# Kernel tuning notes

Hardware: AMD Instinct MI355X
Metric: run time of the kernel (lower is better)

Reference implementation:

```python
import jax, jax.numpy as jnp
import numpy as np

MAX_DEPTH = 9
HIDDEN = 64
EMB = 64
POS_FREQS = 6
IN_C = 1
SIZES = [4 ** d for d in range(MAX_DEPTH + 1)]
OFFSETS = np.concatenate([[0], np.cumsum(SIZES)])  # per-depth slices into concatenated node arrays
TOTAL = int(OFFSETS[-1])  # 349525
POS_DIM = 3 + 2 * POS_FREQS * 3  # 39


def _interleave(v):
    v = v & 0xFFFF
    v = (v | (v << 8)) & 0x00FF00FF
    v = (v | (v << 4)) & 0x0F0F0F0F
    v = (v | (v << 2)) & 0x33333333
    v = (v | (v << 1)) & 0x55555555
    return v


def _deinterleave(v):
    v = v & 0x55555555
    v = (v | (v >> 1)) & 0x33333333
    v = (v | (v >> 2)) & 0x0F0F0F0F
    v = (v | (v >> 4)) & 0x00FF00FF
    v = (v | (v >> 8)) & 0x0000FFFF
    return v


def _xy(d):
    keys = jnp.arange(4 ** d, dtype=jnp.int32)  # full tree: sorted Morton keys = arange
    return _deinterleave(keys), _deinterleave(keys >> 1)


def _neighbors(d):
    # [N, 9] neighbor indices in Morton order grid; -1 outside the image (matches quadtree.neighs padding)
    ix, iy = _xy(d)
    res = 1 << d
    cols = []
    for dy in (-1, 0, 1):
        for dx in (-1, 0, 1):
            nx, ny = ix + dx, iy + dy
            valid = (nx >= 0) & (nx < res) & (ny >= 0) & (ny < res)
            key = _interleave(nx) | (_interleave(ny) << 1)
            cols.append(jnp.where(valid, key, -1))
    return jnp.stack(cols, axis=1)


def _pos_enc(d):
    # node_centers_from_keys + fourier_encode
    ix, iy = _xy(d)
    res = float(1 << d)
    x = (ix.astype(jnp.float32) + 0.5) / res
    y = (iy.astype(jnp.float32) + 0.5) / res
    dn = jnp.full_like(x, float(d) / float(MAX_DEPTH))
    pos = jnp.stack([x, y, dn], axis=1)  # [N, 3]
    freqs = 2.0 ** jnp.arange(POS_FREQS, dtype=jnp.float32)
    ang = pos[:, :, None] * (2.0 * np.pi) * freqs  # [N, 3, F]
    enc = jnp.concatenate([jnp.sin(ang), jnp.cos(ang)], axis=-1).reshape(pos.shape[0], -1)  # [N, 3*2F]
    return jnp.concatenate([pos, enc], axis=1)  # [N, 39]


def setup_inputs() -> dict:
    key = jax.random.key(0)
    ks = jax.random.split(key, 10)
    s = 0.05
    return {
        "features_in": jax.random.normal(ks[0], (TOTAL, IN_C), jnp.float32),
        "in_proj_W": jax.random.normal(ks[1], (IN_C + POS_DIM, HIDDEN), jnp.float32) * s,
        "in_proj_b": jnp.zeros((HIDDEN,), jnp.float32),
        "conv_W": jax.random.normal(ks[2], (MAX_DEPTH + 1, 9 * HIDDEN, HIDDEN), jnp.float32) * s,
        "conv_b": jnp.zeros((MAX_DEPTH + 1, HIDDEN), jnp.float32),
        "emb_W": jax.random.normal(ks[3], (MAX_DEPTH + 1, HIDDEN, EMB), jnp.float32) * s,
        "emb_b": jnp.zeros((MAX_DEPTH + 1, EMB), jnp.float32),
        "ln_g": jnp.ones((MAX_DEPTH + 1, EMB), jnp.float32),
        "ln_b": jnp.zeros((MAX_DEPTH + 1, EMB), jnp.float32),
        "depth_gain": jnp.ones((MAX_DEPTH + 1,), jnp.float32),
    }


def reference(features_in, in_proj_W, in_proj_b, conv_W, conv_b, emb_W, emb_b, ln_g, ln_b, depth_gain):
    D = MAX_DEPTH
    # per-depth input projection with fourier positional encoding
    h = []
    for d in range(D + 1):
        f = features_in[OFFSETS[d]:OFFSETS[d + 1]]
        x = jnp.concatenate([f, _pos_enc(d)], axis=1)  # [N_d, in_c + 39]
        h.append(x @ in_proj_W + in_proj_b)
    # bottom-up: QuadPool (mean over 4 children; full tree => children of parent i are 4i..4i+3) + QuadConv
    for d in range(D, 0, -1):
        Np = 4 ** (d - 1)
        pooled = h[d].reshape(Np, 4, HIDDEN).mean(axis=1)
        hd1 = h[d - 1] + pooled
        if d - 1 >= 1:
            neigh = _neighbors(d - 1)  # [N, 9], -1 at borders
            N = neigh.shape[0]
            padded = jnp.concatenate([hd1, jnp.zeros((1, HIDDEN), hd1.dtype)], axis=0)
            gi = jnp.where(neigh < 0, N, neigh)
            col = padded[gi].reshape(N, 9 * HIDDEN)
            hd1 = jax.nn.relu(col @ conv_W[d - 1] + conv_b[d - 1])
        h[d - 1] = hd1
    # per-depth embedding head: Linear -> LayerNorm -> depth gain
    outs = []
    eps = 1e-5
    for d in range(D + 1):
        z = h[d] @ emb_W[d] + emb_b[d]
        mu = z.mean(-1, keepdims=True)
        var = ((z - mu) ** 2).mean(-1, keepdims=True)
        z = (z - mu) / jnp.sqrt(var + eps) * ln_g[d] + ln_b[d]
        outs.append(depth_gain[d] * z)
    return jnp.concatenate(outs, axis=0)  # [TOTAL, EMB] (E[0]..E[max_depth] concatenated)
```

## Files before the change

kernel.cpp:

```cpp
#include <hip/hip_runtime.h>
#include <hip/hip_bf16.h>

static constexpr int TOTAL = 349525;
static constexpr int OFFS[11] = {0,1,5,21,85,341,1365,5461,21845,87381,349525};
static constexpr size_t CONV_USH = (size_t)8*9*2*4*64*8;
static constexpr size_t EMB_USH  = (size_t)10*2*4*64*8;
static constexpr size_t FRAG_USH = CONV_USH + EMB_USH;
static constexpr size_t FRAG_BYTES = FRAG_USH*2*2;
static constexpr size_t HPRE_BYTES = (size_t)(87381-85)*64*4;
static constexpr int WPREP_BLOCKS = 164;
static constexpr int INPROJ_BLOCKS = (TOTAL + 127)/128;

typedef __attribute__((ext_vector_type(8))) short short8;
typedef __attribute__((ext_vector_type(4))) float f32x4;

__device__ __forceinline__ unsigned deint(unsigned v){
  v &= 0x55555555u;
  v = (v | (v>>1)) & 0x33333333u;
  v = (v | (v>>2)) & 0x0F0F0F0Fu;
  v = (v | (v>>4)) & 0x00FF00FFu;
  v = (v | (v>>8)) & 0x0000FFFFu;
  return v;
}
__device__ __forceinline__ unsigned ileave(unsigned v){
  v &= 0xFFFFu;
  v = (v | (v<<8)) & 0x00FF00FFu;
  v = (v | (v<<4)) & 0x0F0F0F0Fu;
  v = (v | (v<<2)) & 0x33333333u;
  v = (v | (v<<1)) & 0x55555555u;
  return v;
}
__device__ __forceinline__ unsigned short f2bh(float x){
  unsigned u = __float_as_uint(x);
  return (unsigned short)((u + 0x7FFFu + ((u>>16)&1u)) >> 16);
}
__device__ __forceinline__ float bh2f(unsigned short h){
  return __uint_as_float(((unsigned)h) << 16);
}
__device__ __forceinline__ void split8(float4 a, float4 b, short8 &hi, short8 &lo){
  float v[8] = {a.x,a.y,a.z,a.w,b.x,b.y,b.z,b.w};
  unsigned short hv[8], lv[8];
  #pragma unroll
  for (int j=0;j<8;++j){ hv[j]=f2bh(v[j]); lv[j]=f2bh(v[j]-bh2f(hv[j])); }
  hi = short8{(short)hv[0],(short)hv[1],(short)hv[2],(short)hv[3],
              (short)hv[4],(short)hv[5],(short)hv[6],(short)hv[7]};
  lo = short8{(short)lv[0],(short)lv[1],(short)lv[2],(short)lv[3],
              (short)lv[4],(short)lv[5],(short)lv[6],(short)lv[7]};
}

__global__ __launch_bounds__(256) void k_prep(const float* __restrict__ convW,
    const float* __restrict__ embW,
    unsigned short* __restrict__ WH, unsigned short* __restrict__ WLo,
    const float* __restrict__ feat, const float* __restrict__ ipW,
    const float* __restrict__ ipB, float* __restrict__ h,
    float* __restrict__ hpre){
  __shared__ float Alt[128][44];
  __shared__ float Wl[40][68];
  int t = threadIdx.x;
  if ((int)blockIdx.x < WPREP_BLOCKS){
    int tid = blockIdx.x*256 + t;
    if (tid >= 41984) return;
    const float* src;
    size_t dst;
    if (tid < 36864){
      int l=tid&63, cb=(tid>>6)&3, ks=(tid>>8)&1;
      int x=tid>>9; int m=x%9, Lp=x/9;
      int k0=ks*32+((l>>4)<<3), ch=cb*16+(l&15);
      src = convW + (size_t)(Lp+1)*36864 + (size_t)(m*64+k0)*64 + ch;
      dst = (size_t)tid*8;
    } else {
      int t2 = tid - 36864;
      int l=t2&63, cb=(t2>>6)&3, ks=(t2>>8)&1, d=t2>>9;
      int k0=ks*32+((l>>4)<<3), ch=cb*16+(l&15);
      src = embW + (size_t)d*4096 + (size_t)k0*64 + ch;
      dst = CONV_USH + (size_t)t2*8;
    }
    unsigned short hv[8], lv[8];
    #pragma unroll
    for (int j=0;j<8;++j){
      float v = src[(size_t)j*64];
      unsigned short hh = f2bh(v);
      hv[j] = hh;
      lv[j] = f2bh(v - bh2f(hh));
    }
    short8 vh = {(short)hv[0],(short)hv[1],(short)hv[2],(short)hv[3],
                 (short)hv[4],(short)hv[5],(short)hv[6],(short)hv[7]};
    short8 vl = {(short)lv[0],(short)lv[1],(short)lv[2],(short)lv[3],
                 (short)lv[4],(short)lv[5],(short)lv[6],(short)lv[7]};
    *(short8*)(WH  + dst) = vh;
    *(short8*)(WLo + dst) = vl;
    return;
  }
  int base = ((int)blockIdx.x - WPREP_BLOCKS) * 128;
  for (int idx = t; idx < 40*64; idx += 256)
    Wl[idx >> 6][idx & 63] = ipW[idx];
  if (t < 128){
    int g = base + t;
    float* row = Alt[t];
    if (g < TOTAL){
      int d = 0;
      #pragma unroll
      for (int i = 1; i <= 9; ++i) if (g >= OFFS[i]) d = i;
      int local = g - OFFS[d];
      unsigned ix = deint((unsigned)local), iy = deint(((unsigned)local) >> 1);
      float inv = 1.0f / (float)(1 << d);
      float px = ((float)ix + 0.5f) * inv;
      float py = ((float)iy + 0.5f) * inv;
      float pd = (float)d * (1.0f/9.0f);
      row[0] = feat[g]; row[1] = px; row[2] = py; row[3] = pd;
      float p3[3] = {px, py, pd};
      #pragma unroll
      for (int c = 0; c < 3; ++c){
        float s, co;
        __sincosf(6.28318530717958647692f * p3[c], &s, &co);
        float* rb = row + 4 + c*12;
        #pragma unroll
        for (int f = 0; f < 6; ++f){
          rb[f] = s; rb[6+f] = co;
          float s2 = 2.f*s*co, c2 = 1.f - 2.f*s*s;
          s = s2; co = c2;
        }
      }
    } else {
      #pragma unroll
      for (int k = 0; k < 40; ++k) row[k] = 0.f;
    }
  }
  __syncthreads();
  int tr = t >> 3, tc = t & 7;
  float acc[4][8];
  #pragma unroll
  for (int i=0;i<4;++i)
    #pragma unroll
    for (int c=0;c<8;++c) acc[i][c] = 0.f;
  #pragma unroll 2
  for (int k4 = 0; k4 < 10; ++k4){
    float av4[4][4];
    #pragma unroll
    for (int i=0;i<4;++i){
      float4 aa = *(const float4*)&Alt[tr*4+i][k4*4];
      av4[i][0]=aa.x; av4[i][1]=aa.y; av4[i][2]=aa.z; av4[i][3]=aa.w;
    }
    #pragma unroll
    for (int j=0;j<4;++j){
      float4 lo = *(const float4*)&Wl[k4*4+j][tc*8];
      float4 hi = *(const float4*)&Wl[k4*4+j][tc*8+4];
      float wv[8];
      wv[0]=lo.x; wv[1]=lo.y; wv[2]=lo.z; wv[3]=lo.w;
      wv[4]=hi.x; wv[5]=hi.y; wv[6]=hi.z; wv[7]=hi.w;
      #pragma unroll
      for (int i=0;i<4;++i){
        float a = av4[i][j];
        #pragma unroll
        for (int c=0;c<8;++c) acc[i][c] += a*wv[c];
      }
    }
  }
  #pragma unroll
  for (int i=0;i<4;++i){
    int g = base + tr*4 + i;
    if (g >= TOTAL) continue;
    float ov[8];
    #pragma unroll
    for (int c=0;c<8;++c) ov[c] = acc[i][c] + ipB[tc*8+c];
    float* dst = &h[(size_t)g*64 + tc*8];
    *(float4*)dst       = *(const float4*)&ov[0];
    *(float4*)(dst + 4) = *(const float4*)&ov[4];
    if (hpre && g >= OFFS[4] && g < OFFS[9]){
      float* dp = hpre + (size_t)(g - OFFS[4])*64 + tc*8;
      *(float4*)dp       = *(const float4*)&ov[0];
      *(float4*)(dp + 4) = *(const float4*)&ov[4];
    }
  }
}

__device__ __forceinline__ void conv_dev(float* __restrict__ h,
    const float* __restrict__ hPar,
    const unsigned short* __restrict__ WHl, const unsigned short* __restrict__ WLl,
    const float* __restrict__ Bb, int N, int offL, int offC, int lbits, int bnum,
    unsigned short* haloH, unsigned short* haloL, int* hkey, int t){
  int nb = bnum * 64;
  int res = 1 << lbits;
  if (t < 100){
    int i = t % 10, j = t / 10;
    int gx = (int)deint((unsigned)nb) - 1 + i;
    int gy = (int)deint(((unsigned)nb)>>1) - 1 + j;
    bool ok = (gx>=0 && gy>=0 && gx<res && gy<res);
    hkey[t] = ok ? (int)(ileave((unsigned)gx) | (ileave((unsigned)gy)<<1)) : -1;
  }
  __syncthreads();
  const float* hC = h + (size_t)offC*64;
  for (int e = t; e < 1600; e += 256){
    int hi_ = e >> 4, u = e & 15;
    int key = hkey[hi_];
    float4 r = make_float4(0.f,0.f,0.f,0.f);
    if (key >= 0){
      const float4* c = (const float4*)(hC + (size_t)(4*key)*64) + u;
      float4 c0 = c[0], c1 = c[16], c2 = c[32], c3 = c[48];
      float4 pr = *((const float4*)(hPar + (size_t)key*64) + u);
      r.x = 0.25f*(c0.x+c1.x+c2.x+c3.x) + pr.x;
      r.y = 0.25f*(c0.y+c1.y+c2.y+c3.y) + pr.y;
      r.z = 0.25f*(c0.z+c1.z+c2.z+c3.z) + pr.z;
      r.w = 0.25f*(c0.w+c1.w+c2.w+c3.w) + pr.w;
    }
    unsigned short h0=f2bh(r.x), h1=f2bh(r.y), h2=f2bh(r.z), h3=f2bh(r.w);
    *(ushort4*)&haloH[hi_*72 + u*4] = make_ushort4(h0,h1,h2,h3);
    *(ushort4*)&haloL[hi_*72 + u*4] = make_ushort4(
        f2bh(r.x - bh2f(h0)), f2bh(r.y - bh2f(h1)),
        f2bh(r.z - bh2f(h2)), f2bh(r.w - bh2f(h3)));
  }
  __syncthreads();
  int cb   = __builtin_amdgcn_readfirstlane(t >> 6);
  int lane = t & 63;
  int q = lane >> 4;
  int chl = cb*16 + (lane & 15);
  int lx0,ly0,lx1,ly1,lx2,ly2,lx3,ly3;
  {
    int n0 = (lane&15), n1 = 16+(lane&15), n2 = 32+(lane&15), n3 = 48+(lane&15);
    lx0=(int)deint((unsigned)n0); ly0=(int)deint(((unsigned)n0)>>1);
    lx1=(int)deint((unsigned)n1); ly1=(int)deint(((unsigned)n1)>>1);
    lx2=(int)deint((unsigned)n2); ly2=(int)deint(((unsigned)n2)>>1);
    lx3=(int)deint((unsigned)n3); ly3=(int)deint(((unsigned)n3)>>1);
  }
  f32x4 acc0 = {0.f,0.f,0.f,0.f}, acc1 = acc0, acc2 = acc0, acc3 = acc0;
  #pragma unroll 1
  for (int dy=0;dy<3;++dy){
    #pragma unroll 1
    for (int dx=0;dx<3;++dx){
      int m = dy*3 + dx;
      int r0 = (ly0+dy)*10 + lx0+dx;
      int r1 = (ly1+dy)*10 + lx1+dx;
      int r2 = (ly2+dy)*10 + lx2+dx;
      int r3 = (ly3+dy)*10 + lx3+dx;
      #pragma unroll
      for (int ks=0;ks<2;++ks){
        const unsigned short* fp = WHl + ((size_t)((m*2+ks)*4 + cb)*64 + lane)*8;
        const unsigned short* fq = WLl + ((size_t)((m*2+ks)*4 + cb)*64 + lane)*8;
        short8 bh = *(const short8*)fp;
        short8 bl = *(const short8*)fq;
        int so = (ks*4 + q)*8;
        short8 ah0 = *(const short8*)&haloH[r0*72 + so];
        short8 al0 = *(const short8*)&haloL[r0*72 + so];
        short8 ah1 = *(const short8*)&haloH[r1*72 + so];
        short8 al1 = *(const short8*)&haloL[r1*72 + so];
        short8 ah2 = *(const short8*)&haloH[r2*72 + so];
        short8 al2 = *(const short8*)&haloL[r2*72 + so];
        short8 ah3 = *(const short8*)&haloH[r3*72 + so];
        short8 al3 = *(const short8*)&haloL[r3*72 + so];
        acc0 = __builtin_amdgcn_mfma_f32_16x16x32_bf16(ah0, bh, acc0, 0,0,0);
        acc1 = __builtin_amdgcn_mfma_f32_16x16x32_bf16(ah1, bh, acc1, 0,0,0);
        acc2 = __builtin_amdgcn_mfma_f32_16x16x32_bf16(ah2, bh, acc2, 0,0,0);
        acc3 = __builtin_amdgcn_mfma_f32_16x16x32_bf16(ah3, bh, acc3, 0,0,0);
        acc0 = __builtin_amdgcn_mfma_f32_16x16x32_bf16(al0, bh, acc0, 0,0,0);
        acc1 = __builtin_amdgcn_mfma_f32_16x16x32_bf16(al1, bh, acc1, 0,0,0);
        acc2 = __builtin_amdgcn_mfma_f32_16x16x32_bf16(al2, bh, acc2, 0,0,0);
        acc3 = __builtin_amdgcn_mfma_f32_16x16x32_bf16(al3, bh, acc3, 0,0,0);
        acc0 = __builtin_amdgcn_mfma_f32_16x16x32_bf16(ah0, bl, acc0, 0,0,0);
        acc1 = __builtin_amdgcn_mfma_f32_16x16x32_bf16(ah1, bl, acc1, 0,0,0);
        acc2 = __builtin_amdgcn_mfma_f32_16x16x32_bf16(ah2, bl, acc2, 0,0,0);
        acc3 = __builtin_amdgcn_mfma_f32_16x16x32_bf16(ah3, bl, acc3, 0,0,0);
      }
    }
  }
  float bias = Bb[chl];
  int rowb = q*4;
  float* hO = h + (size_t)(offL + nb)*64;
  #pragma unroll
  for (int reg=0;reg<4;++reg){
    int n0 = rowb + reg;
    float v0 = acc0[reg] + bias; if (nb + n0      < N) hO[(size_t)(n0     )*64 + chl] = v0 > 0.f ? v0 : 0.f;
    float v1 = acc1[reg] + bias; if (nb + n0 + 16 < N) hO[(size_t)(n0 + 16)*64 + chl] = v1 > 0.f ? v1 : 0.f;
    float v2 = acc2[reg] + bias; if (nb + n0 + 32 < N) hO[(size_t)(n0 + 32)*64 + chl] = v2 > 0.f ? v2 : 0.f;
    float v3 = acc3[reg] + bias; if (nb + n0 + 48 < N) hO[(size_t)(n0 + 48)*64 + chl] = v3 > 0.f ? v3 : 0.f;
  }
}

__device__ __forceinline__ void emb_tile(float* __restrict__ h,
    const unsigned short* __restrict__ EH, const unsigned short* __restrict__ ELo,
    const float* __restrict__ embB, const float* __restrict__ lng,
    const float* __restrict__ lnb, const float* __restrict__ gain,
    int d, size_t rowbase, int validN, int lane){
  int q = lane >> 4, li = lane & 15;
  const float* rp = h + (rowbase + li)*64 + q*8;
  float4 a0 = *(const float4*)rp;
  float4 a1 = *(const float4*)(rp + 4);
  float4 a2 = *(const float4*)(rp + 32);
  float4 a3 = *(const float4*)(rp + 36);
  short8 ah0, al0, ah1, al1;
  split8(a0, a1, ah0, al0);
  split8(a2, a3, ah1, al1);
  f32x4 acc0 = {0.f,0.f,0.f,0.f}, acc1 = acc0, acc2 = acc0, acc3 = acc0;
  #define EMB_CB(CB, ACC) { \
    size_t f0 = (((size_t)(d*2+0)*4 + (CB))*64 + lane)*8; \
    size_t f1 = (((size_t)(d*2+1)*4 + (CB))*64 + lane)*8; \
    short8 bh0 = *(const short8*)(EH + f0); \
    short8 bl0 = *(const short8*)(ELo + f0); \
    short8 bh1 = *(const short8*)(EH + f1); \
    short8 bl1 = *(const short8*)(ELo + f1); \
    ACC = __builtin_amdgcn_mfma_f32_16x16x32_bf16(ah0, bh0, ACC, 0,0,0); \
    ACC = __builtin_amdgcn_mfma_f32_16x16x32_bf16(al0, bh0, ACC, 0,0,0); \
    ACC = __builtin_amdgcn_mfma_f32_16x16x32_bf16(ah0, bl0, ACC, 0,0,0); \
    ACC = __builtin_amdgcn_mfma_f32_16x16x32_bf16(ah1, bh1, ACC, 0,0,0); \
    ACC = __builtin_amdgcn_mfma_f32_16x16x32_bf16(al1, bh1, ACC, 0,0,0); \
    ACC = __builtin_amdgcn_mfma_f32_16x16x32_bf16(ah1, bl1, ACC, 0,0,0); }
  EMB_CB(0, acc0)
  EMB_CB(1, acc1)
  EMB_CB(2, acc2)
  EMB_CB(3, acc3)
  #undef EMB_CB
  float b0 = embB[d*64 +      li];
  float b1 = embB[d*64 + 16 + li];
  float b2 = embB[d*64 + 32 + li];
  float b3 = embB[d*64 + 48 + li];
  float mu[4], rs[4];
  float z0[4], z1[4], z2[4], z3[4];
  #pragma unroll
  for (int r=0;r<4;++r){
    z0[r] = acc0[r] + b0;
    z1[r] = acc1[r] + b1;
    z2[r] = acc2[r] + b2;
    z3[r] = acc3[r] + b3;
    float s  = z0[r] + z1[r] + z2[r] + z3[r];
    float qv = z0[r]*z0[r] + z1[r]*z1[r] + z2[r]*z2[r] + z3[r]*z3[r];
    #pragma unroll
    for (int mk=1; mk<16; mk<<=1){
      s  += __shfl_xor(s, mk, 64);
      qv += __shfl_xor(qv, mk, 64);
    }
    float m = s * 0.015625f;
    mu[r] = m;
    rs[r] = rsqrtf(qv * 0.015625f - m*m + 1e-5f);
  }
  float g0 = lng[d*64 +      li], l0 = lnb[d*64 +      li];
  float g1 = lng[d*64 + 16 + li], l1 = lnb[d*64 + 16 + li];
  float g2 = lng[d*64 + 32 + li], l2 = lnb[d*64 + 32 + li];
  float g3 = lng[d*64 + 48 + li], l3 = lnb[d*64 + 48 + li];
  float gn = gain[d];
  #pragma unroll
  for (int r=0;r<4;++r){
    int ni = q*4 + r;
    if (ni < validN){
      float* row = h + (rowbase + ni)*64;
      row[     li] = ((z0[r] - mu[r])*rs[r]*g0 + l0)*gn;
      row[16 + li] = ((z1[r] - mu[r])*rs[r]*g1 + l1)*gn;
      row[32 + li] = ((z2[r] - mu[r])*rs[r]*g2 + l2)*gn;
      row[48 + li] = ((z3[r] - mu[r])*rs[r]*g3 + l3)*gn;
    }
  }
}
__device__ __forceinline__ void emb128(float* h,
    const unsigned short* EH, const unsigned short* ELo, const float* embB,
    const float* lng, const float* lnb, const float* gain,
    int d, int blk, int t){
  int w = t >> 6, lane = t & 63;
  size_t base = (size_t)OFFS[d] + (size_t)blk*128;
  emb_tile(h, EH, ELo, embB, lng, lnb, gain, d, base + (size_t)w*16,      16, lane);
  emb_tile(h, EH, ELo, embB, lng, lnb, gain, d, base + (size_t)(w+4)*16, 16, lane);
}

__global__ __launch_bounds__(256) void k_conv_emb(float* __restrict__ h,
    const float* __restrict__ hPar,
    const unsigned short* __restrict__ WHl, const unsigned short* __restrict__ WLl,
    const float* __restrict__ Bb, int N, int offL, int offC, int lbits, int NC,
    const unsigned short* __restrict__ EH, const unsigned short* __restrict__ ELo,
    const float* __restrict__ embB, const float* __restrict__ lng,
    const float* __restrict__ lnb, const float* __restrict__ gain, int embD){
  __shared__ unsigned short haloH[100*72];
  __shared__ unsigned short haloL[100*72];
  __shared__ int hkey[100];
  int t = threadIdx.x;
  if ((int)blockIdx.x >= NC){
    emb128(h, EH, ELo, embB, lng, lnb, gain, embD, blockIdx.x - NC, t);
    return;
  }
  conv_dev(h, hPar, WHl, WLl, Bb, N, offL, offC, lbits, blockIdx.x,
           haloH, haloL, hkey, t);
}

template<int L>
__device__ __forceinline__ void tail_level256(float* __restrict__ h,
    const unsigned short* __restrict__ WHc, const unsigned short* __restrict__ WLc,
    const float* __restrict__ convB, const float* __restrict__ Hpar,
    unsigned short* __restrict__ PtH, unsigned short* __restrict__ PtL, int t){
  constexpr int Np  = 1 << (2*L);
  constexpr int NTt = (Np + 15)/16;
  constexpr int res = 1 << L;
  int cb = __builtin_amdgcn_readfirstlane(t >> 6);
  int lane = t & 63;
  int q = lane >> 4, li = lane & 15;
  int chl = cb*16 + li;
  int lx[NTt], ly[NTt];
  #pragma unroll
  for (int i=0;i<NTt;++i){
    unsigned n = (unsigned)(i*16 + li);
    lx[i] = (int)deint(n); ly[i] = (int)deint(n >> 1);
  }
  f32x4 acc[NTt];
  #pragma unroll
  for (int i=0;i<NTt;++i) acc[i] = f32x4{0.f,0.f,0.f,0.f};
  short8 bh0, bl0, bh1, bl1;
  {
    size_t f0 = ((size_t)(0*4 + cb)*64 + lane)*8;
    size_t f1 = ((size_t)(1*4 + cb)*64 + lane)*8;
    bh0 = *(const short8*)(WHc + f0); bl0 = *(const short8*)(WLc + f0);
    bh1 = *(const short8*)(WHc + f1); bl1 = *(const short8*)(WLc + f1);
  }
  #pragma unroll 1
  for (int m=0;m<9;++m){
    short8 nh0, nl0, nh1, nl1;
    if (m < 8){
      size_t f0 = ((size_t)(((m+1)*2+0)*4 + cb)*64 + lane)*8;
      size_t f1 = ((size_t)(((m+1)*2+1)*4 + cb)*64 + lane)*8;
      nh0 = *(const short8*)(WHc + f0); nl0 = *(const short8*)(WLc + f0);
      nh1 = *(const short8*)(WHc + f1); nl1 = *(const short8*)(WLc + f1);
    }
    int dy = m/3 - 1, dx = m%3 - 1;
    #pragma unroll
    for (int i=0;i<NTt;++i){
      int nx = lx[i]+dx, ny = ly[i]+dy;
      int key = (nx>=0 && ny>=0 && nx<res && ny<res)
              ? (int)(ileave((unsigned)nx) | (ileave((unsigned)ny)<<1)) : Np;
      const unsigned short* pH = PtH + key*72;
      const unsigned short* pL = PtL + key*72;
      short8 ah0 = *(const short8*)(pH + q*8);
      short8 al0 = *(const short8*)(pL + q*8);
      short8 ah1 = *(const short8*)(pH + 32 + q*8);
      short8 al1 = *(const short8*)(pL + 32 + q*8);
      acc[i] = __builtin_amdgcn_mfma_f32_16x16x32_bf16(ah0, bh0, acc[i], 0,0,0);
      acc[i] = __builtin_amdgcn_mfma_f32_16x16x32_bf16(al0, bh0, acc[i], 0,0,0);
      acc[i] = __builtin_amdgcn_mfma_f32_16x16x32_bf16(ah0, bl0, acc[i], 0,0,0);
      acc[i] = __builtin_amdgcn_mfma_f32_16x16x32_bf16(ah1, bh1, acc[i], 0,0,0);
      acc[i] = __builtin_amdgcn_mfma_f32_16x16x32_bf16(al1, bh1, acc[i], 0,0,0);
      acc[i] = __builtin_amdgcn_mfma_f32_16x16x32_bf16(ah1, bl1, acc[i], 0,0,0);
    }
    if (m < 8){ bh0 = nh0; bl0 = nl0; bh1 = nh1; bl1 = nl1; }
  }
  float bias = convB[L*64 + chl];
  float vq[NTt][4];
  #pragma unroll
  for (int i=0;i<NTt;++i){
    #pragma unroll
    for (int reg=0;reg<4;++reg){
      int ni = i*16 + q*4 + reg;
      float v = acc[i][reg] + bias;
      v = v > 0.f ? v : 0.f;
      vq[i][reg] = v;
      if (ni < Np) h[(size_t)(OFFS[L] + ni)*64 + chl] = v;
    }
  }
  __syncthreads();
  if (L > 1){
    constexpr int Pp = Np/4;
    #pragma unroll
    for (int i=0;i<NTt;++i){
      int p = i*4 + q;
      if (p < Pp){
        float pooled = 0.25f*(vq[i][0]+vq[i][1]+vq[i][2]+vq[i][3])
                     + Hpar[(size_t)(OFFS[L-1] + p)*64 + chl];
        unsigned short hh = f2bh(pooled);
        PtH[p*72 + chl] = hh;
        PtL[p*72 + chl] = f2bh(pooled - bh2f(hh));
      }
    }
    if (t < 64){ PtH[Pp*72 + t] = 0; PtL[Pp*72 + t] = 0; }
  } else {
    if (q == 0){
      float pooled = 0.25f*(vq[0][0]+vq[0][1]+vq[0][2]+vq[0][3]) + Hpar[chl];
      h[chl] = pooled;
    }
  }
  __syncthreads();
}

__device__ __forceinline__ void do_tail_phase(int b, float* __restrict__ h,
    const unsigned short* WH, const unsigned short* WLo, const float* convB,
    const unsigned short* EH, const unsigned short* ELo, const float* embB,
    const float* lng, const float* lnb, const float* gain,
    unsigned short* PtH, unsigned short* PtL, float* Hpar, int t){
  int w = t >> 6, lane = t & 63;
  if (b != 0){
    if (b < 9) emb128(h, EH, ELo, embB, lng, lnb, gain, 5, b-1, t);
    return;
  }
  for (int e = t; e < 21*16; e += 256)
    ((float4*)Hpar)[e] = ((const float4*)h)[e];
  for (int e = t; e < 65*16; e += 256){
    int node = e >> 4, u = e & 15;
    float4 r = make_float4(0.f,0.f,0.f,0.f);
    if (node < 64){
      const float4* c = (const float4*)(h + (size_t)(OFFS[4] + 4*node)*64) + u;
      float4 c0 = c[0], c1 = c[16], c2 = c[32], c3 = c[48];
      float4 pr = *((const float4*)(h + (size_t)(OFFS[3] + node)*64) + u);
      r.x = 0.25f*(c0.x+c1.x+c2.x+c3.x) + pr.x;
      r.y = 0.25f*(c0.y+c1.y+c2.y+c3.y) + pr.y;
      r.z = 0.25f*(c0.z+c1.z+c2.z+c3.z) + pr.z;
      r.w = 0.25f*(c0.w+c1.w+c2.w+c3.w) + pr.w;
    }
    unsigned short h0=f2bh(r.x), h1=f2bh(r.y), h2=f2bh(r.z), h3=f2bh(r.w);
    *(ushort4*)&PtH[node*72 + u*4] = make_ushort4(h0,h1,h2,h3);
    *(ushort4*)&PtL[node*72 + u*4] = make_ushort4(
        f2bh(r.x - bh2f(h0)), f2bh(r.y - bh2f(h1)),
        f2bh(r.z - bh2f(h2)), f2bh(r.w - bh2f(h3)));
  }
  __syncthreads();
  tail_level256<3>(h, WH + (size_t)2*36864, WLo + (size_t)2*36864, convB, Hpar, PtH, PtL, t);
  tail_level256<2>(h, WH + (size_t)1*36864, WLo + (size_t)1*36864, convB, Hpar, PtH, PtL, t);
  tail_level256<1>(h, WH,                   WLo,                   convB, Hpar, PtH, PtL, t);
  for (int j = w; j < 23; j += 4){
    int d, tile;
    if (j < 16)      { d=4; tile=j;    }
    else if (j < 20) { d=3; tile=j-16; }
    else if (j == 20){ d=2; tile=0;    }
    else if (j == 21){ d=1; tile=0;    }
    else             { d=0; tile=0;    }
    int Nlev = 1 << (2*d);
    int valid = Nlev - tile*16;
    emb_tile(h, EH, ELo, embB, lng, lnb, gain, d,
             (size_t)OFFS[d] + (size_t)tile*16, valid > 16 ? 16 : valid, lane);
  }
}

__global__ __launch_bounds__(256) void k_tailonly(float* __restrict__ h,
    const unsigned short* __restrict__ WH, const unsigned short* __restrict__ WLo,
    const float* __restrict__ convB,
    const unsigned short* __restrict__ EH, const unsigned short* __restrict__ ELo,
    const float* __restrict__ embB, const float* __restrict__ lng,
    const float* __restrict__ lnb, const float* __restrict__ gain){
  __shared__ __align__(16) char smem[24128];
  unsigned short* PtH = (unsigned short*)smem;
  unsigned short* PtL = (unsigned short*)(smem + 9360);
  float* Hpar = (float*)(smem + 18720);
  do_tail_phase(blockIdx.x, h, WH, WLo, convB, EH, ELo, embB, lng, lnb, gain,
                PtH, PtL, Hpar, threadIdx.x);
}

extern "C" void kernel_launch(void* const* d_in, const int* in_sizes, int n_in,
                              void* d_out, int out_size, void* d_ws, size_t ws_size,
                              hipStream_t stream) {
  (void)in_sizes; (void)n_in; (void)out_size;
  const float* feat  = (const float*)d_in[0];
  const float* ipW   = (const float*)d_in[1];
  const float* ipB   = (const float*)d_in[2];
  const float* convW = (const float*)d_in[3];
  const float* convB = (const float*)d_in[4];
  const float* embW  = (const float*)d_in[5];
  const float* embB  = (const float*)d_in[6];
  const float* lng   = (const float*)d_in[7];
  const float* lnb   = (const float*)d_in[8];
  const float* gain  = (const float*)d_in[9];
  float* h = (float*)d_out;

  unsigned short* WH  = (unsigned short*)d_ws;
  unsigned short* WLo = WH + FRAG_USH;
  const unsigned short* EH  = WH  + CONV_USH;
  const unsigned short* ELo = WLo + CONV_USH;
  float* hpre = (ws_size >= FRAG_BYTES + HPRE_BYTES)
              ? (float*)((char*)d_ws + FRAG_BYTES) : nullptr;

  k_prep<<<WPREP_BLOCKS + INPROJ_BLOCKS, 256, 0, stream>>>(
      convW, embW, WH, WLo, feat, ipW, ipB, h, hpre);

  for (int L = 8; L >= 4; --L){
    int Np = 1 << (2*L);
    int NC = Np/64;
    int embD = (L <= 7) ? L + 2 : -1;
    int embBlocks = (embD > 0) ? (1 << (2*embD)) / 128 : 0;
    const float* hPar = hpre ? (hpre + (size_t)(OFFS[L] - OFFS[4])*64)
                             : (h + (size_t)OFFS[L]*64);
    k_conv_emb<<<NC + embBlocks, 256, 0, stream>>>(h, hPar,
        WH  + (size_t)(L-1)*36864, WLo + (size_t)(L-1)*36864,
        convB + (size_t)L*64, Np, OFFS[L], OFFS[L+1], L, NC,
        EH, ELo, embB, lng, lnb, gain, embD);
  }

  k_tailonly<<<9, 256, 0, stream>>>(h, WH, WLo, convB,
      EH, ELo, embB, lng, lnb, gain);
}
```

Before: 206.9 us.

## Move embedding-head blocks for depths 6-9 into final tail kernel for overlap

Embedding-head blocks for depths 6-9 used to ride along with the per-level conv launches. They now all run as extra blocks in the final kernel, next to the 9 blocks that do the serial tail phase. The conv launches become conv-only. The large, independent embedding work is meant to fill the GPU while the tail phase's few blocks leave most compute units idle. The trade-off is that the earlier conv launches lose their own overlap with embedding work, and the final launch becomes much larger.

```diff
diff --git a/kernel.cpp b/kernel.cpp
--- a/kernel.cpp
+++ b/kernel.cpp
@@ -273,6 +273,17 @@
     float v2 = acc2[reg] + bias; if (nb + n0 + 32 < N) hO[(size_t)(n0 + 32)*64 + chl] = v2 > 0.f ? v2 : 0.f;
     float v3 = acc3[reg] + bias; if (nb + n0 + 48 < N) hO[(size_t)(n0 + 48)*64 + chl] = v3 > 0.f ? v3 : 0.f;
   }
+}
+
+__global__ __launch_bounds__(256) void k_conv(float* __restrict__ h,
+    const float* __restrict__ hPar,
+    const unsigned short* __restrict__ WHl, const unsigned short* __restrict__ WLl,
+    const float* __restrict__ Bb, int N, int offL, int offC, int lbits){
+  __shared__ unsigned short haloH[100*72];
+  __shared__ unsigned short haloL[100*72];
+  __shared__ int hkey[100];
+  conv_dev(h, hPar, WHl, WLl, Bb, N, offL, offC, lbits, blockIdx.x,
+           haloH, haloL, hkey, threadIdx.x);
 }
 
 __device__ __forceinline__ void emb_tile(float* __restrict__ h,
@@ -358,25 +369,6 @@
   emb_tile(h, EH, ELo, embB, lng, lnb, gain, d, base + (size_t)(w+4)*16, 16, lane);
 }
 
-__global__ __launch_bounds__(256) void k_conv_emb(float* __restrict__ h,
-    const float* __restrict__ hPar,
-    const unsigned short* __restrict__ WHl, const unsigned short* __restrict__ WLl,
-    const float* __restrict__ Bb, int N, int offL, int offC, int lbits, int NC,
-    const unsigned short* __restrict__ EH, const unsigned short* __restrict__ ELo,
-    const float* __restrict__ embB, const float* __restrict__ lng,
-    const float* __restrict__ lnb, const float* __restrict__ gain, int embD){
-  __shared__ unsigned short haloH[100*72];
-  __shared__ unsigned short haloL[100*72];
-  __shared__ int hkey[100];
-  int t = threadIdx.x;
-  if ((int)blockIdx.x >= NC){
-    emb128(h, EH, ELo, embB, lng, lnb, gain, embD, blockIdx.x - NC, t);
-    return;
-  }
-  conv_dev(h, hPar, WHl, WLl, Bb, N, offL, offC, lbits, blockIdx.x,
-           haloH, haloL, hkey, t);
-}
-
 template<int L>
 __device__ __forceinline__ void tail_level256(float* __restrict__ h,
     const unsigned short* __restrict__ WHc, const unsigned short* __restrict__ WLc,
@@ -520,7 +512,7 @@
   }
 }
 
-__global__ __launch_bounds__(256) void k_tailonly(float* __restrict__ h,
+__global__ __launch_bounds__(256) void k_final(float* __restrict__ h,
     const unsigned short* __restrict__ WH, const unsigned short* __restrict__ WLo,
     const float* __restrict__ convB,
     const unsigned short* __restrict__ EH, const unsigned short* __restrict__ ELo,
@@ -530,8 +522,20 @@
   unsigned short* PtH = (unsigned short*)smem;
   unsigned short* PtL = (unsigned short*)(smem + 9360);
   float* Hpar = (float*)(smem + 18720);
-  do_tail_phase(blockIdx.x, h, WH, WLo, convB, EH, ELo, embB, lng, lnb, gain,
-                PtH, PtL, Hpar, threadIdx.x);
+  int t = threadIdx.x;
+  int b = blockIdx.x;
+  if (b >= 9){
+    int bb = b - 9;
+    int d, blk;
+    if      (bb < 2048){ d = 9; blk = bb;        }
+    else if (bb < 2560){ d = 8; blk = bb - 2048; }
+    else if (bb < 2688){ d = 7; blk = bb - 2560; }
+    else               { d = 6; blk = bb - 2688; }
+    emb128(h, EH, ELo, embB, lng, lnb, gain, d, blk, t);
+    return;
+  }
+  do_tail_phase(b, h, WH, WLo, convB, EH, ELo, embB, lng, lnb, gain,
+                PtH, PtL, Hpar, t);
 }
 
 extern "C" void kernel_launch(void* const* d_in, const int* in_sizes, int n_in,
@@ -562,17 +566,13 @@
 
   for (int L = 8; L >= 4; --L){
     int Np = 1 << (2*L);
-    int NC = Np/64;
-    int embD = (L <= 7) ? L + 2 : -1;
-    int embBlocks = (embD > 0) ? (1 << (2*embD)) / 128 : 0;
     const float* hPar = hpre ? (hpre + (size_t)(OFFS[L] - OFFS[4])*64)
                              : (h + (size_t)OFFS[L]*64);
-    k_conv_emb<<<NC + embBlocks, 256, 0, stream>>>(h, hPar,
+    k_conv<<<Np/64, 256, 0, stream>>>(h, hPar,
         WH  + (size_t)(L-1)*36864, WLo + (size_t)(L-1)*36864,
-        convB + (size_t)L*64, Np, OFFS[L], OFFS[L+1], L, NC,
-        EH, ELo, embB, lng, lnb, gain, embD);
-  }
-
-  k_tailonly<<<9, 256, 0, stream>>>(h, WH, WLo, convB,
+        convB + (size_t)L*64, Np, OFFS[L], OFFS[L+1], L);
+  }
+
+  k_final<<<9 + 2720, 256, 0, stream>>>(h, WH, WLo, convB,
       EH, ELo, embB, lng, lnb, gain);
 }
```

Measured after the change: 193.3 us. 1.07x faster.
